# Kernel tuning notes

Hardware: AMD Instinct MI355X
Metric: run time of the kernel (lower is better)

Reference implementation:

```python
import jax, jax.numpy as jnp
import numpy as np

B, S, H, DFF, E, K = 2, 2048, 1024, 2048, 8, 2


def setup_inputs() -> dict:
    key = jax.random.key(0)
    ks = jax.random.split(key, 8)
    sc_h = 1.0 / np.sqrt(H)
    sc_f = 1.0 / np.sqrt(DFF)
    x = jax.random.normal(ks[0], (B, S, H), dtype=jnp.float32)
    Wg = jax.random.uniform(ks[1], (E, H), jnp.float32, -sc_h, sc_h)  # gate (no bias)
    W1 = jax.random.uniform(ks[2], (E, DFF, H), jnp.float32, -sc_h, sc_h)  # SiGLU gate proj
    b1 = jax.random.uniform(ks[3], (E, DFF), jnp.float32, -sc_h, sc_h)
    W2 = jax.random.uniform(ks[4], (E, DFF, H), jnp.float32, -sc_h, sc_h)  # SiGLU value proj
    b2 = jax.random.uniform(ks[5], (E, DFF), jnp.float32, -sc_h, sc_h)
    W3 = jax.random.uniform(ks[6], (E, H, DFF), jnp.float32, -sc_f, sc_f)  # down proj
    b3 = jax.random.uniform(ks[7], (E, H), jnp.float32, -sc_f, sc_f)
    return {"x": x, "Wg": Wg, "W1": W1, "b1": b1, "W2": W2, "b2": b2, "W3": W3, "b3": b3}


def _moe(x, Wg, W1, b1, W2, b2, W3, b3):
    Bm, Sm, Hm = x.shape
    xt = x.reshape(-1, Hm)  # [T, H]
    gout = xt @ Wg.T  # [T, E]
    topv, topi = jax.lax.top_k(gout, K)  # [T, K]
    w = jax.nn.softmax(topv, axis=-1)  # [T, K]
    # combine weights per expert: comb[t, e] = sum_k w[t,k] * 1[topi[t,k]==e]
    comb = jnp.einsum('tke,tk->te', jax.nn.one_hot(topi, E, dtype=x.dtype), w)  # [T, E]
    # dense per-expert FFN (fixed-shape equivalent of the gather/scatter loop)
    g = jnp.einsum('th,efh->etf', xt, W1) + b1[:, None, :]  # [E, T, DFF]
    v = jnp.einsum('th,efh->etf', xt, W2) + b2[:, None, :]
    h = jax.nn.silu(g) * v  # SiGLU
    eo = jnp.einsum('etf,ehf->eth', h, W3) + b3[:, None, :]  # [E, T, H]
    out = jnp.einsum('eth,te->th', eo, comb)
    return out.reshape(Bm, Sm, Hm)


def reference(x, Wg, W1, b1, W2, b2, W3, b3):
    return _moe(x, Wg, W1, b1, W2, b2, W3, b3)
```

## Files before the change

### kernel.cpp

```cpp
#include <hip/hip_runtime.h>
#include <hip/hip_bf16.h>

#define T_TOK 4096
#define H_DIM 1024
#define DFF_D 2048
#define E_NUM 8
#define K_TOP 2
#define KSPLIT 2
#define MAXJOBS 136

typedef __attribute__((ext_vector_type(8))) short s16x8;
typedef __attribute__((ext_vector_type(4))) float f32x4;

__device__ __forceinline__ ushort f2bf(float f) {
    unsigned u = __float_as_uint(f);
    u = (u + 0x7FFFu + ((u >> 16) & 1u)) >> 16;
    return (ushort)u;
}

__device__ __forceinline__ void glds16(const ushort* g, ushort* l) {
    __builtin_amdgcn_global_load_lds(
        (const __attribute__((address_space(1))) unsigned*)g,
        (__attribute__((address_space(3))) unsigned*)l, 16, 0, 0);
}

__device__ __forceinline__ s16x8 lds_frag(const ushort* base, int row, int bytecol) {
    int byte = row * 128 + (bytecol ^ ((row & 7) << 4));
    return *(const s16x8*)((const char*)base + byte);
}

__device__ __forceinline__ void cvt8(const float* p, ushort* dst, size_t i) {
    float4 a = ((const float4*)(p + i * 8))[0];
    float4 b = ((const float4*)(p + i * 8))[1];
    union { ushort us[8]; uint4 q; } o;
    o.us[0] = f2bf(a.x); o.us[1] = f2bf(a.y); o.us[2] = f2bf(a.z); o.us[3] = f2bf(a.w);
    o.us[4] = f2bf(b.x); o.us[5] = f2bf(b.y); o.us[6] = f2bf(b.z); o.us[7] = f2bf(b.w);
    ((uint4*)dst)[i] = o.q;
}

__global__ __launch_bounds__(256) void cvt_kernel(
    const float* __restrict__ in, ushort* __restrict__ out, int n8)
{
    int i = blockIdx.x * blockDim.x + threadIdx.x;
    const int stride = gridDim.x * blockDim.x;
    for (; i < n8; i += stride) cvt8(in, out, i);
}

__global__ __launch_bounds__(256) void cvt3_kernel(
    const float* __restrict__ x,  ushort* __restrict__ xbf,
    const float* __restrict__ W1, ushort* __restrict__ w1bf,
    const float* __restrict__ W2, ushort* __restrict__ w2bf)
{
    const int nW = E_NUM * DFF_D * H_DIM / 8;
    const int nX = T_TOK * H_DIM / 8;
    const int total = 2 * nW + nX;
    int i = blockIdx.x * blockDim.x + threadIdx.x;
    const int stride = gridDim.x * blockDim.x;
    for (; i < total; i += stride) {
        if (i < nW)            cvt8(W1, w1bf, i);
        else if (i < 2 * nW)   cvt8(W2, w2bf, i - nW);
        else                   cvt8(x,  xbf,  i - 2 * nW);
    }
}

__global__ __launch_bounds__(256) void gate_kernel(
    const float* __restrict__ x, const float* __restrict__ Wg,
    int* __restrict__ topi_packed, float* __restrict__ wt_slot)
{
    const int t = blockIdx.x * 4 + (threadIdx.x >> 6);
    const int lane = threadIdx.x & 63;
    const float* xr = x + (size_t)t * H_DIM;
    float xv[16];
    #pragma unroll
    for (int j = 0; j < 16; ++j) xv[j] = xr[j * 64 + lane];

    float score[E_NUM];
    #pragma unroll
    for (int e = 0; e < E_NUM; ++e) {
        const float* wr = Wg + e * H_DIM;
        float p = 0.f;
        #pragma unroll
        for (int j = 0; j < 16; ++j) p += xv[j] * wr[j * 64 + lane];
        #pragma unroll
        for (int s = 32; s >= 1; s >>= 1) p += __shfl_xor(p, s, 64);
        score[e] = p;
    }
    if (lane == 0) {
        int i0 = 0;
        #pragma unroll
        for (int e = 1; e < E_NUM; ++e) if (score[e] > score[i0]) i0 = e;
        int i1 = (i0 == 0) ? 1 : 0;
        #pragma unroll
        for (int e = 0; e < E_NUM; ++e)
            if (e != i0 && score[e] > score[i1]) i1 = e;
        float e1 = expf(score[i1] - score[i0]);
        float w0 = 1.f / (1.f + e1);
        float w1 = e1 / (1.f + e1);
        topi_packed[t] = i0 | (i1 << 8);
        wt_slot[t * K_TOP + 0] = w0;
        wt_slot[t * K_TOP + 1] = w1;
    }
}

__global__ __launch_bounds__(256) void build_lists(
    const int* __restrict__ topi_packed,
    int* __restrict__ cnt, int* __restrict__ tok_list, int* __restrict__ slot_list)
{
    const int e = blockIdx.x;
    __shared__ int lcnt;
    if (threadIdx.x == 0) lcnt = 0;
    __syncthreads();
    for (int t = threadIdx.x; t < T_TOK; t += 256) {
        int pk = topi_packed[t];
        int i0 = pk & 0xff;
        int i1 = (pk >> 8) & 0xff;
        if (i0 == e) {
            int p = atomicAdd(&lcnt, 1);
            tok_list[e * T_TOK + p] = t;
            slot_list[e * T_TOK + p] = t * K_TOP + 0;
        }
        if (i1 == e) {
            int p = atomicAdd(&lcnt, 1);
            tok_list[e * T_TOK + p] = t;
            slot_list[e * T_TOK + p] = t * K_TOP + 1;
        }
    }
    __syncthreads();
    if (threadIdx.x == 0) cnt[e] = lcnt;
}

__global__ void build_jobs(const int* __restrict__ cnt,
                           int* __restrict__ jobs, int* __restrict__ njobs)
{
    if (threadIdx.x == 0 && blockIdx.x == 0) {
        int n = 0;
        for (int e = 0; e < E_NUM; ++e) {
            int mt = (cnt[e] + 63) >> 6;
            for (int m = 0; m < mt; ++m) jobs[n++] = (e << 16) | m;
        }
        njobs[0] = n;
    }
}

__global__ __launch_bounds__(256) void up_kernel(
    const ushort* __restrict__ xbf,
    const ushort* __restrict__ w1bf, const float* __restrict__ b1,
    const ushort* __restrict__ w2bf, const float* __restrict__ b2,
    const int* __restrict__ cnt, const int* __restrict__ tok_list,
    const int* __restrict__ slot_list, const float* __restrict__ wt_slot,
    const int* __restrict__ jobs, const int* __restrict__ njobs,
    ushort* __restrict__ h)
{
    if ((int)blockIdx.y >= njobs[0]) return;
    const int jb = jobs[blockIdx.y];
    const int e = jb >> 16;
    const int mbase = (jb & 0xffff) * 64;
    const int M = cnt[e];
    const int nbase = blockIdx.x * 64;
    const int tid = threadIdx.x;
    const int lane = tid & 63;
    const int w = tid >> 6;

    __shared__ ushort As[64 * 64];
    __shared__ ushort B1s[64 * 64];
    __shared__ ushort B2s[64 * 64];

    const ushort* srcA[2];
    const ushort* srcB1[2];
    const ushort* srcB2[2];
    #pragma unroll
    for (int j = 0; j < 2; ++j) {
        int o = j * 4096 + tid * 16;
        int r = o >> 7;
        int cb = (o & 127) ^ ((r & 7) << 4);
        int lpos = mbase + r; if (lpos > M - 1) lpos = M - 1;
        int tok = tok_list[e * T_TOK + lpos];
        srcA[j]  = xbf + (size_t)tok * H_DIM + (cb >> 1);
        srcB1[j] = w1bf + ((size_t)e * DFF_D + nbase + r) * H_DIM + (cb >> 1);
        srcB2[j] = w2bf + ((size_t)e * DFF_D + nbase + r) * H_DIM + (cb >> 1);
    }

    const f32x4 zero = {0.f, 0.f, 0.f, 0.f};
    f32x4 accg[4], accv[4];
    #pragma unroll
    for (int ni = 0; ni < 4; ++ni) { accg[ni] = zero; accv[ni] = zero; }

    const int r16 = lane & 15;
    const int g4  = lane >> 4;
    const int cb0 = g4 * 16;

    for (int k0 = 0; k0 < H_DIM; k0 += 64) {
        #pragma unroll
        for (int j = 0; j < 2; ++j) {
            glds16(srcA[j]  + k0, &As[j * 2048 + w * 512]);
            glds16(srcB1[j] + k0, &B1s[j * 2048 + w * 512]);
            glds16(srcB2[j] + k0, &B2s[j * 2048 + w * 512]);
        }
        __syncthreads();
        #pragma unroll
        for (int kk = 0; kk < 2; ++kk) {
            s16x8 af = lds_frag(As, w * 16 + r16, kk * 64 + cb0);
            #pragma unroll
            for (int ni = 0; ni < 4; ++ni) {
                s16x8 bf1 = lds_frag(B1s, ni * 16 + r16, kk * 64 + cb0);
                s16x8 bf2 = lds_frag(B2s, ni * 16 + r16, kk * 64 + cb0);
                accg[ni] = __builtin_amdgcn_mfma_f32_16x16x32_bf16(af, bf1, accg[ni], 0, 0, 0);
                accv[ni] = __builtin_amdgcn_mfma_f32_16x16x32_bf16(af, bf2, accv[ni], 0, 0, 0);
            }
        }
        __syncthreads();
    }

    #pragma unroll
    for (int j = 0; j < 4; ++j) {
        int p = mbase + w * 16 + g4 * 4 + j;
        if (p < M) {
            int slot = slot_list[e * T_TOK + p];
            float wgt = wt_slot[slot];
            #pragma unroll
            for (int ni = 0; ni < 4; ++ni) {
                int col = nbase + ni * 16 + r16;
                float g = accg[ni][j] + b1[e * DFF_D + col];
                float v = accv[ni][j] + b2[e * DFF_D + col];
                float s = g / (1.f + __expf(-g));
                h[(size_t)slot * DFF_D + col] = f2bf(wgt * s * v);
            }
        }
    }
}

__global__ __launch_bounds__(256) void down_kernel(
    const ushort* __restrict__ h,
    const ushort* __restrict__ w3bf, const float* __restrict__ b3,
    const int* __restrict__ cnt, const int* __restrict__ slot_list,
    const float* __restrict__ wt_slot,
    const int* __restrict__ jobs, const int* __restrict__ njobs,
    float* __restrict__ out)
{
    if ((int)blockIdx.y >= njobs[0]) return;
    const int jb = jobs[blockIdx.y];
    const int e = jb >> 16;
    const int mbase = (jb & 0xffff) * 64;
    const int M = cnt[e];
    const int nt = blockIdx.x >> 1;
    const int kc = blockIdx.x & 1;
    const int nbase = nt * 128;
    const int tid = threadIdx.x;
    const int lane = tid & 63;
    const int w = tid >> 6;

    __shared__ ushort As[64 * 64];
    __shared__ ushort Bs[128 * 64];

    const int kbeg = kc * (DFF_D / KSPLIT);
    const ushort* srcA[2];
    const ushort* srcB[4];
    #pragma unroll
    for (int j = 0; j < 2; ++j) {
        int o = j * 4096 + tid * 16;
        int r = o >> 7;
        int cb = (o & 127) ^ ((r & 7) << 4);
        int lpos = mbase + r; if (lpos > M - 1) lpos = M - 1;
        int slot = slot_list[e * T_TOK + lpos];
        srcA[j] = h + (size_t)slot * DFF_D + kbeg + (cb >> 1);
    }
    #pragma unroll
    for (int j = 0; j < 4; ++j) {
        int o = j * 4096 + tid * 16;
        int r = o >> 7;
        int cb = (o & 127) ^ ((r & 7) << 4);
        srcB[j] = w3bf + ((size_t)e * H_DIM + nbase + r) * DFF_D + kbeg + (cb >> 1);
    }

    const f32x4 zero = {0.f, 0.f, 0.f, 0.f};
    f32x4 acc[8];
    #pragma unroll
    for (int ni = 0; ni < 8; ++ni) acc[ni] = zero;

    const int r16 = lane & 15;
    const int g4  = lane >> 4;
    const int cb0 = g4 * 16;

    for (int k0 = 0; k0 < DFF_D / KSPLIT; k0 += 64) {
        #pragma unroll
        for (int j = 0; j < 2; ++j)
            glds16(srcA[j] + k0, &As[j * 2048 + w * 512]);
        #pragma unroll
        for (int j = 0; j < 4; ++j)
            glds16(srcB[j] + k0, &Bs[j * 2048 + w * 512]);
        __syncthreads();
        #pragma unroll
        for (int kk = 0; kk < 2; ++kk) {
            s16x8 af = lds_frag(As, w * 16 + r16, kk * 64 + cb0);
            #pragma unroll
            for (int ni = 0; ni < 8; ++ni) {
                s16x8 bf = lds_frag(Bs, ni * 16 + r16, kk * 64 + cb0);
                acc[ni] = __builtin_amdgcn_mfma_f32_16x16x32_bf16(af, bf, acc[ni], 0, 0, 0);
            }
        }
        __syncthreads();
    }

    #pragma unroll
    for (int j = 0; j < 4; ++j) {
        int p = mbase + w * 16 + g4 * 4 + j;
        if (p < M) {
            int slot = slot_list[e * T_TOK + p];
            float wgt = wt_slot[slot];
            int t2 = slot >> 1;
            #pragma unroll
            for (int ni = 0; ni < 8; ++ni) {
                int col = nbase + ni * 16 + r16;
                float v = acc[ni][j];
                if (kc == 0) v += wgt * b3[e * H_DIM + col];
                atomicAdd(&out[(size_t)t2 * H_DIM + col], v);
            }
        }
    }
}

extern "C" void kernel_launch(void* const* d_in, const int* in_sizes, int n_in,
                              void* d_out, int out_size, void* d_ws, size_t ws_size,
                              hipStream_t stream) {
    const float* x  = (const float*)d_in[0];
    const float* Wg = (const float*)d_in[1];
    const float* W1 = (const float*)d_in[2];
    const float* b1 = (const float*)d_in[3];
    const float* W2 = (const float*)d_in[4];
    const float* b2 = (const float*)d_in[5];
    const float* W3 = (const float*)d_in[6];
    const float* b3 = (const float*)d_in[7];
    float* out = (float*)d_out;

    char* ws = (char*)d_ws;
    int*   cnt       = (int*)(ws);
    int*   njobs     = (int*)(ws + 128);
    int*   jobs      = (int*)(ws + 256);
    int*   tok_list  = (int*)(ws + 1024);
    int*   slot_list = (int*)(ws + 1024 + E_NUM * T_TOK * 4);
    float* wt_slot   = (float*)(ws + 1024 + 2 * E_NUM * T_TOK * 4);
    int*   topi      = (int*)(ws + 320 * 1024);
    ushort* xbf  = (ushort*)(ws + (size_t)1  * (1u << 20));
    ushort* w1bf = (ushort*)(ws + (size_t)16 * (1u << 20));
    ushort* w2bf = (ushort*)(ws + (size_t)48 * (1u << 20));
    ushort* hbuf = (ushort*)(ws + (size_t)80 * (1u << 20));
    ushort* w3bf = w1bf;

    hipMemsetAsync(d_out, 0, (size_t)T_TOK * H_DIM * sizeof(float), stream);

    cvt3_kernel<<<2048, 256, 0, stream>>>(x, xbf, W1, w1bf, W2, w2bf);

    gate_kernel<<<T_TOK / 4, 256, 0, stream>>>(x, Wg, topi, wt_slot);
    build_lists<<<E_NUM, 256, 0, stream>>>(topi, cnt, tok_list, slot_list);
    build_jobs<<<1, 64, 0, stream>>>(cnt, jobs, njobs);

    dim3 gup(DFF_D / 64, MAXJOBS);
    up_kernel<<<gup, 256, 0, stream>>>(xbf, w1bf, b1, w2bf, b2, cnt, tok_list,
                                       slot_list, wt_slot, jobs, njobs, hbuf);

    cvt_kernel<<<2048, 256, 0, stream>>>(W3, w3bf, E_NUM * H_DIM * DFF_D / 8);

    dim3 gdn((H_DIM / 128) * KSPLIT, MAXJOBS);
    down_kernel<<<gdn, 256, 0, stream>>>(hbuf, w3bf, b3, cnt, slot_list, wt_slot,
                                         jobs, njobs, out);
}
```

Before: 283.4 us.

## Enlarge up-proj M tile and replace atomic down-proj scatter with combine kernel

The up-projection now processes 128 tokens per block instead of 64, reusing each loaded W1/W2 tile across twice as many rows and halving weight traffic. The down-projection drops its K split and atomic adds into out, writing per-slot expert outputs in bf16 instead. A new combine kernel sums the two slots per token and adds the bias. This also removes the output memset. The costs are an extra kernel, a bf16 intermediate that loses some precision, and fewer blocks in the down-projection.

After: 260.4 us. 1.09x faster.

```diff
diff --git a/kernel.cpp b/kernel.cpp
--- a/kernel.cpp
+++ b/kernel.cpp
@@ -6,8 +6,8 @@
 #define DFF_D 2048
 #define E_NUM 8
 #define K_TOP 2
-#define KSPLIT 2
-#define MAXJOBS 136
+#define MAXJOBS64 136
+#define MAXJOBS128 72
 
 typedef __attribute__((ext_vector_type(8))) short s16x8;
 typedef __attribute__((ext_vector_type(4))) float f32x4;
@@ -16,6 +16,10 @@
     unsigned u = __float_as_uint(f);
     u = (u + 0x7FFFu + ((u >> 16) & 1u)) >> 16;
     return (ushort)u;
+}
+
+__device__ __forceinline__ float bf2f(short s) {
+    return __uint_as_float(((unsigned)(ushort)s) << 16);
 }
 
 __device__ __forceinline__ void glds16(const ushort* g, ushort* l) {
@@ -130,15 +134,19 @@
 }
 
 __global__ void build_jobs(const int* __restrict__ cnt,
-                           int* __restrict__ jobs, int* __restrict__ njobs)
+                           int* __restrict__ jobs64, int* __restrict__ jobs128,
+                           int* __restrict__ njobs)
 {
     if (threadIdx.x == 0 && blockIdx.x == 0) {
-        int n = 0;
+        int n = 0, n2 = 0;
         for (int e = 0; e < E_NUM; ++e) {
             int mt = (cnt[e] + 63) >> 6;
-            for (int m = 0; m < mt; ++m) jobs[n++] = (e << 16) | m;
+            for (int m = 0; m < mt; ++m) jobs64[n++] = (e << 16) | m;
+            int mt2 = (cnt[e] + 127) >> 7;
+            for (int m = 0; m < mt2; ++m) jobs128[n2++] = (e << 16) | m;
         }
         njobs[0] = n;
+        njobs[1] = n2;
     }
 }
 
@@ -148,42 +156,50 @@
     const ushort* __restrict__ w2bf, const float* __restrict__ b2,
     const int* __restrict__ cnt, const int* __restrict__ tok_list,
     const int* __restrict__ slot_list, const float* __restrict__ wt_slot,
-    const int* __restrict__ jobs, const int* __restrict__ njobs,
+    const int* __restrict__ jobs128, const int* __restrict__ njobs,
     ushort* __restrict__ h)
 {
-    if ((int)blockIdx.y >= njobs[0]) return;
-    const int jb = jobs[blockIdx.y];
+    if ((int)blockIdx.y >= njobs[1]) return;
+    const int jb = jobs128[blockIdx.y];
     const int e = jb >> 16;
-    const int mbase = (jb & 0xffff) * 64;
+    const int mbase = (jb & 0xffff) * 128;
     const int M = cnt[e];
     const int nbase = blockIdx.x * 64;
     const int tid = threadIdx.x;
     const int lane = tid & 63;
     const int w = tid >> 6;
 
-    __shared__ ushort As[64 * 64];
+    __shared__ ushort As[128 * 64];
     __shared__ ushort B1s[64 * 64];
     __shared__ ushort B2s[64 * 64];
 
-    const ushort* srcA[2];
+    const ushort* srcA[4];
     const ushort* srcB1[2];
     const ushort* srcB2[2];
     #pragma unroll
-    for (int j = 0; j < 2; ++j) {
+    for (int j = 0; j < 4; ++j) {
         int o = j * 4096 + tid * 16;
         int r = o >> 7;
         int cb = (o & 127) ^ ((r & 7) << 4);
         int lpos = mbase + r; if (lpos > M - 1) lpos = M - 1;
         int tok = tok_list[e * T_TOK + lpos];
-        srcA[j]  = xbf + (size_t)tok * H_DIM + (cb >> 1);
+        srcA[j] = xbf + (size_t)tok * H_DIM + (cb >> 1);
+    }
+    #pragma unroll
+    for (int j = 0; j < 2; ++j) {
+        int o = j * 4096 + tid * 16;
+        int r = o >> 7;
+        int cb = (o & 127) ^ ((r & 7) << 4);
         srcB1[j] = w1bf + ((size_t)e * DFF_D + nbase + r) * H_DIM + (cb >> 1);
         srcB2[j] = w2bf + ((size_t)e * DFF_D + nbase + r) * H_DIM + (cb >> 1);
     }
 
     const f32x4 zero = {0.f, 0.f, 0.f, 0.f};
-    f32x4 accg[4], accv[4];
-    #pragma unroll
-    for (int ni = 0; ni < 4; ++ni) { accg[ni] = zero; accv[ni] = zero; }
+    f32x4 accg[2][4], accv[2][4];
+    #pragma unroll
+    for (int mi = 0; mi < 2; ++mi)
+        #pragma unroll
+        for (int ni = 0; ni < 4; ++ni) { accg[mi][ni] = zero; accv[mi][ni] = zero; }
 
     const int r16 = lane & 15;
     const int g4  = lane >> 4;
@@ -191,39 +207,51 @@
 
     for (int k0 = 0; k0 < H_DIM; k0 += 64) {
         #pragma unroll
+        for (int j = 0; j < 4; ++j)
+            glds16(srcA[j] + k0, &As[j * 2048 + (tid >> 3) * 64 + (tid & 7) * 8]);
+        #pragma unroll
         for (int j = 0; j < 2; ++j) {
-            glds16(srcA[j]  + k0, &As[j * 2048 + w * 512]);
-            glds16(srcB1[j] + k0, &B1s[j * 2048 + w * 512]);
-            glds16(srcB2[j] + k0, &B2s[j * 2048 + w * 512]);
+            glds16(srcB1[j] + k0, &B1s[j * 2048 + (tid >> 3) * 64 + (tid & 7) * 8]);
+            glds16(srcB2[j] + k0, &B2s[j * 2048 + (tid >> 3) * 64 + (tid & 7) * 8]);
         }
         __syncthreads();
         #pragma unroll
         for (int kk = 0; kk < 2; ++kk) {
-            s16x8 af = lds_frag(As, w * 16 + r16, kk * 64 + cb0);
+            s16x8 bf1[4], bf2[4];
             #pragma unroll
             for (int ni = 0; ni < 4; ++ni) {
-                s16x8 bf1 = lds_frag(B1s, ni * 16 + r16, kk * 64 + cb0);
-                s16x8 bf2 = lds_frag(B2s, ni * 16 + r16, kk * 64 + cb0);
-                accg[ni] = __builtin_amdgcn_mfma_f32_16x16x32_bf16(af, bf1, accg[ni], 0, 0, 0);
-                accv[ni] = __builtin_amdgcn_mfma_f32_16x16x32_bf16(af, bf2, accv[ni], 0, 0, 0);
+                bf1[ni] = lds_frag(B1s, ni * 16 + r16, kk * 64 + cb0);
+                bf2[ni] = lds_frag(B2s, ni * 16 + r16, kk * 64 + cb0);
             }
+            #pragma unroll
+            for (int mi = 0; mi < 2; ++mi) {
+                s16x8 af = lds_frag(As, w * 32 + mi * 16 + r16, kk * 64 + cb0);
+                #pragma unroll
+                for (int ni = 0; ni < 4; ++ni) {
+                    accg[mi][ni] = __builtin_amdgcn_mfma_f32_16x16x32_bf16(af, bf1[ni], accg[mi][ni], 0, 0, 0);
+                    accv[mi][ni] = __builtin_amdgcn_mfma_f32_16x16x32_bf16(af, bf2[ni], accv[mi][ni], 0, 0, 0);
+                }
+            }
         }
         __syncthreads();
     }
 
     #pragma unroll
-    for (int j = 0; j < 4; ++j) {
-        int p = mbase + w * 16 + g4 * 4 + j;
-        if (p < M) {
-            int slot = slot_list[e * T_TOK + p];
-            float wgt = wt_slot[slot];
-            #pragma unroll
-            for (int ni = 0; ni < 4; ++ni) {
-                int col = nbase + ni * 16 + r16;
-                float g = accg[ni][j] + b1[e * DFF_D + col];
-                float v = accv[ni][j] + b2[e * DFF_D + col];
-                float s = g / (1.f + __expf(-g));
-                h[(size_t)slot * DFF_D + col] = f2bf(wgt * s * v);
+    for (int mi = 0; mi < 2; ++mi) {
+        #pragma unroll
+        for (int j = 0; j < 4; ++j) {
+            int p = mbase + w * 32 + mi * 16 + g4 * 4 + j;
+            if (p < M) {
+                int slot = slot_list[e * T_TOK + p];
+                float wgt = wt_slot[slot];
+                #pragma unroll
+                for (int ni = 0; ni < 4; ++ni) {
+                    int col = nbase + ni * 16 + r16;
+                    float g = accg[mi][ni][j] + b1[e * DFF_D + col];
+                    float v = accv[mi][ni][j] + b2[e * DFF_D + col];
+                    float s = g / (1.f + __expf(-g));
+                    h[(size_t)slot * DFF_D + col] = f2bf(wgt * s * v);
+                }
             }
         }
     }
@@ -231,20 +259,17 @@
 
 __global__ __launch_bounds__(256) void down_kernel(
     const ushort* __restrict__ h,
-    const ushort* __restrict__ w3bf, const float* __restrict__ b3,
+    const ushort* __restrict__ w3bf,
     const int* __restrict__ cnt, const int* __restrict__ slot_list,
-    const float* __restrict__ wt_slot,
-    const int* __restrict__ jobs, const int* __restrict__ njobs,
-    float* __restrict__ out)
+    const int* __restrict__ jobs64, const int* __restrict__ njobs,
+    ushort* __restrict__ eo)
 {
     if ((int)blockIdx.y >= njobs[0]) return;
-    const int jb = jobs[blockIdx.y];
+    const int jb = jobs64[blockIdx.y];
     const int e = jb >> 16;
     const int mbase = (jb & 0xffff) * 64;
     const int M = cnt[e];
-    const int nt = blockIdx.x >> 1;
-    const int kc = blockIdx.x & 1;
-    const int nbase = nt * 128;
+    const int nbase = blockIdx.x * 128;
     const int tid = threadIdx.x;
     const int lane = tid & 63;
     const int w = tid >> 6;
@@ -252,7 +277,6 @@
     __shared__ ushort As[64 * 64];
     __shared__ ushort Bs[128 * 64];
 
-    const int kbeg = kc * (DFF_D / KSPLIT);
     const ushort* srcA[2];
     const ushort* srcB[4];
     #pragma unroll
@@ -262,14 +286,14 @@
         int cb = (o & 127) ^ ((r & 7) << 4);
         int lpos = mbase + r; if (lpos > M - 1) lpos = M - 1;
         int slot = slot_list[e * T_TOK + lpos];
-        srcA[j] = h + (size_t)slot * DFF_D + kbeg + (cb >> 1);
+        srcA[j] = h + (size_t)slot * DFF_D + (cb >> 1);
     }
     #pragma unroll
     for (int j = 0; j < 4; ++j) {
         int o = j * 4096 + tid * 16;
         int r = o >> 7;
         int cb = (o & 127) ^ ((r & 7) << 4);
-        srcB[j] = w3bf + ((size_t)e * H_DIM + nbase + r) * DFF_D + kbeg + (cb >> 1);
+        srcB[j] = w3bf + ((size_t)e * H_DIM + nbase + r) * DFF_D + (cb >> 1);
     }
 
     const f32x4 zero = {0.f, 0.f, 0.f, 0.f};
@@ -281,13 +305,13 @@
     const int g4  = lane >> 4;
     const int cb0 = g4 * 16;
 
-    for (int k0 = 0; k0 < DFF_D / KSPLIT; k0 += 64) {
+    for (int k0 = 0; k0 < DFF_D; k0 += 64) {
         #pragma unroll
         for (int j = 0; j < 2; ++j)
-            glds16(srcA[j] + k0, &As[j * 2048 + w * 512]);
+            glds16(srcA[j] + k0, &As[j * 2048 + (tid >> 3) * 64 + (tid & 7) * 8]);
         #pragma unroll
         for (int j = 0; j < 4; ++j)
-            glds16(srcB[j] + k0, &Bs[j * 2048 + w * 512]);
+            glds16(srcB[j] + k0, &Bs[j * 2048 + (tid >> 3) * 64 + (tid & 7) * 8]);
         __syncthreads();
         #pragma unroll
         for (int kk = 0; kk < 2; ++kk) {
@@ -306,17 +330,44 @@
         int p = mbase + w * 16 + g4 * 4 + j;
         if (p < M) {
             int slot = slot_list[e * T_TOK + p];
-            float wgt = wt_slot[slot];
-            int t2 = slot >> 1;
             #pragma unroll
             for (int ni = 0; ni < 8; ++ni) {
                 int col = nbase + ni * 16 + r16;
-                float v = acc[ni][j];
-                if (kc == 0) v += wgt * b3[e * H_DIM + col];
-                atomicAdd(&out[(size_t)t2 * H_DIM + col], v);
+                eo[(size_t)slot * H_DIM + col] = f2bf(acc[ni][j]);
             }
         }
     }
+}
+
+__global__ __launch_bounds__(256) void combine_kernel(
+    const ushort* __restrict__ eo, const int* __restrict__ topi_packed,
+    const float* __restrict__ wt_slot, const float* __restrict__ b3,
+    float* __restrict__ out)
+{
+    const int i = blockIdx.x * 256 + threadIdx.x;
+    const int t = i >> 7;
+    const int c0 = (i & 127) * 8;
+    const int pk = topi_packed[t];
+    const int e0 = pk & 0xff, e1 = (pk >> 8) & 0xff;
+    const float w0 = wt_slot[2 * t], w1 = wt_slot[2 * t + 1];
+    s16x8 a = *(const s16x8*)(eo + (size_t)(2 * t) * H_DIM + c0);
+    s16x8 b = *(const s16x8*)(eo + (size_t)(2 * t + 1) * H_DIM + c0);
+    const float4* p0 = (const float4*)(b3 + e0 * H_DIM + c0);
+    const float4* p1 = (const float4*)(b3 + e1 * H_DIM + c0);
+    float4 b0a = p0[0], b0b = p0[1];
+    float4 b1a = p1[0], b1b = p1[1];
+    float4 r0, r1;
+    r0.x = bf2f(a[0]) + bf2f(b[0]) + w0 * b0a.x + w1 * b1a.x;
+    r0.y = bf2f(a[1]) + bf2f(b[1]) + w0 * b0a.y + w1 * b1a.y;
+    r0.z = bf2f(a[2]) + bf2f(b[2]) + w0 * b0a.z + w1 * b1a.z;
+    r0.w = bf2f(a[3]) + bf2f(b[3]) + w0 * b0a.w + w1 * b1a.w;
+    r1.x = bf2f(a[4]) + bf2f(b[4]) + w0 * b0b.x + w1 * b1b.x;
+    r1.y = bf2f(a[5]) + bf2f(b[5]) + w0 * b0b.y + w1 * b1b.y;
+    r1.z = bf2f(a[6]) + bf2f(b[6]) + w0 * b0b.z + w1 * b1b.z;
+    r1.w = bf2f(a[7]) + bf2f(b[7]) + w0 * b0b.w + w1 * b1b.w;
+    float4* op = (float4*)(out + (size_t)t * H_DIM + c0);
+    op[0] = r0;
+    op[1] = r1;
 }
 
 extern "C" void kernel_launch(void* const* d_in, const int* in_sizes, int n_in,
@@ -334,8 +385,9 @@
 
     char* ws = (char*)d_ws;
     int*   cnt       = (int*)(ws);
-    int*   njobs     = (int*)(ws + 128);
-    int*   jobs      = (int*)(ws + 256);
+    int*   njobs     = (int*)(ws + 64);
+    int*   jobs64    = (int*)(ws + 128);
+    int*   jobs128   = (int*)(ws + 704);
     int*   tok_list  = (int*)(ws + 1024);
     int*   slot_list = (int*)(ws + 1024 + E_NUM * T_TOK * 4);
     float* wt_slot   = (float*)(ws + 1024 + 2 * E_NUM * T_TOK * 4);
@@ -344,23 +396,24 @@
     ushort* w1bf = (ushort*)(ws + (size_t)16 * (1u << 20));
     ushort* w2bf = (ushort*)(ws + (size_t)48 * (1u << 20));
     ushort* hbuf = (ushort*)(ws + (size_t)80 * (1u << 20));
-    ushort* w3bf = w1bf;
-
-    hipMemsetAsync(d_out, 0, (size_t)T_TOK * H_DIM * sizeof(float), stream);
+    ushort* w3bf = w2bf;
+    ushort* eobf = w1bf;
 
     cvt3_kernel<<<2048, 256, 0, stream>>>(x, xbf, W1, w1bf, W2, w2bf);
 
     gate_kernel<<<T_TOK / 4, 256, 0, stream>>>(x, Wg, topi, wt_slot);
     build_lists<<<E_NUM, 256, 0, stream>>>(topi, cnt, tok_list, slot_list);
-    build_jobs<<<1, 64, 0, stream>>>(cnt, jobs, njobs);
-
-    dim3 gup(DFF_D / 64, MAXJOBS);
+    build_jobs<<<1, 64, 0, stream>>>(cnt, jobs64, jobs128, njobs);
+
+    dim3 gup(DFF_D / 64, MAXJOBS128);
     up_kernel<<<gup, 256, 0, stream>>>(xbf, w1bf, b1, w2bf, b2, cnt, tok_list,
-                                       slot_list, wt_slot, jobs, njobs, hbuf);
+                                       slot_list, wt_slot, jobs128, njobs, hbuf);
 
     cvt_kernel<<<2048, 256, 0, stream>>>(W3, w3bf, E_NUM * H_DIM * DFF_D / 8);
 
-    dim3 gdn((H_DIM / 128) * KSPLIT, MAXJOBS);
-    down_kernel<<<gdn, 256, 0, stream>>>(hbuf, w3bf, b3, cnt, slot_list, wt_slot,
-                                         jobs, njobs, out);
-}
+    dim3 gdn(H_DIM / 128, MAXJOBS64);
+    down_kernel<<<gdn, 256, 0, stream>>>(hbuf, w3bf, cnt, slot_list,
+                                         jobs64, njobs, eobf);
+
+    combine_kernel<<<T_TOK * H_DIM / 8 / 256, 256, 0, stream>>>(eobf, topi, wt_slot, b3, out);
+}
```
